# Kernel tuning notes

Measured on AMD Instinct MI355X. Metric: run time of the kernel, lower is better.

## Reference

```python
import jax, jax.numpy as jnp
import numpy as np

N, K, B, D, T = 30000, 32, 8, 256, 10
NC = T + 1            # int_small_classes
LB_COL, UB_COL = 21, 22
INF = 1e18


def _ln(x, g, b, eps=1e-5):
    m = jnp.mean(x, axis=-1, keepdims=True)
    v = jnp.mean((x - m) ** 2, axis=-1, keepdims=True)
    return (x - m) * jax.lax.rsqrt(v + eps) * g + b


def _head(x, ng, nb, W1, b1, W2, b2, Wh, bh):
    # LayerNorm -> Linear -> GELU -> Linear -> GELU -> residual -> head (dropout off: eval)
    h = _ln(x, ng, nb)
    h = jax.nn.gelu(h @ W1.T + b1, approximate=False)
    h = jax.nn.gelu(h @ W2.T + b2, approximate=False)
    return (x + h) @ Wh.T + bh


def setup_inputs():
    key = jax.random.key(0)
    ks = jax.random.split(key, 32)
    s = 0.05
    inp = {}
    inp['evolved_tokens'] = jax.random.normal(ks[0], (B * K, D), jnp.float32)
    inp['var_batch'] = jnp.sort(jax.random.randint(ks[1], (N,), 0, B))
    aw = jax.random.uniform(ks[2], (N, K), jnp.float32)
    inp['attn_weights'] = aw / aw.sum(-1, keepdims=True)
    inp['var_types'] = jax.random.randint(ks[3], (N,), 0, 3)
    inp['z_var_0'] = jax.random.normal(ks[4], (N, D), jnp.float32)
    vf = 0.1 * jax.random.normal(ks[5], (N, 23), jnp.float32)
    lb = jnp.floor(jax.random.uniform(ks[6], (N,), minval=-5.0, maxval=0.0))
    ub = lb + jnp.floor(jax.random.uniform(ks[7], (N,), minval=0.0, maxval=30.0))
    ub = jnp.where(jax.random.uniform(ks[8], (N,)) < 0.1, 1e19, ub)
    inp['variable_features'] = vf.at[:, LB_COL].set(lb).at[:, UB_COL].set(ub)
    # deslice proj + fusion norm
    inp['Wp'] = s * jax.random.normal(ks[9], (D, D), jnp.float32)
    inp['bp'] = jnp.zeros((D,), jnp.float32)
    inp['fn_g'] = jnp.ones((D,), jnp.float32)
    inp['fn_b'] = jnp.zeros((D,), jnp.float32)
    # three decoder heads
    i = 10
    for name, out in (('bin', 1), ('ints', NC), ('intl', 1)):
        inp[name + '_ng'] = jnp.ones((D,), jnp.float32)
        inp[name + '_nb'] = jnp.zeros((D,), jnp.float32)
        inp[name + '_W1'] = s * jax.random.normal(ks[i], (D, D), jnp.float32)
        inp[name + '_b1'] = jnp.zeros((D,), jnp.float32)
        inp[name + '_W2'] = s * jax.random.normal(ks[i + 1], (D, D), jnp.float32)
        inp[name + '_b2'] = jnp.zeros((D,), jnp.float32)
        inp[name + '_Wh'] = s * jax.random.normal(ks[i + 2], (out, D), jnp.float32)
        inp[name + '_bh'] = (jnp.full((out,), -0.5, jnp.float32) if name == 'bin'
                             else jnp.zeros((out,), jnp.float32))
        i += 3
    return inp


def reference(evolved_tokens, var_batch, attn_weights, var_types, z_var_0,
              variable_features, Wp, bp, fn_g, fn_b,
              bin_ng, bin_nb, bin_W1, bin_b1, bin_W2, bin_b2, bin_Wh, bin_bh,
              ints_ng, ints_nb, ints_W1, ints_b1, ints_W2, ints_b2, ints_Wh, ints_bh,
              intl_ng, intl_nb, intl_W1, intl_b1, intl_W2, intl_b2, intl_Wh, intl_bh):
    # 1. deslice: attn_weights @ projected evolved tokens of the variable's graph
    proj = evolved_tokens @ Wp.T + bp          # [B*K, D]
    tok3 = proj.reshape(B, K, D)
    z_des = jnp.einsum('nk,nkd->nd', attn_weights, tok3[var_batch])  # [N, D]
    # 2. residual fusion + LayerNorm
    z_out = _ln(z_des + z_var_0, fn_g, fn_b)
    # 3. routing (extract_int_routing)
    lb = variable_features[:, LB_COL]
    ub = variable_features[:, UB_COL]
    is_int = var_types == 2
    finite = (jnp.abs(lb) < INF) & (jnp.abs(ub) < INF)
    mask_int_small = is_int & finite & ((ub - lb) <= T)
    mask_int_large = is_int & ~mask_int_small
    mask_bin = var_types == 1
    offsets = jnp.floor(lb)                                   # [N]
    ranges = jnp.clip(jnp.ceil(ub) - offsets + 1.0, 1.0, NC).astype(jnp.int32)  # [N]
    # 4. decode. Heads are evaluated densely on all N rows; the original's
    #    gather->MLP->scatter equals row-selection of these dense outputs.
    prob_bin = jax.nn.sigmoid(_head(z_out, bin_ng, bin_nb, bin_W1, bin_b1,
                                    bin_W2, bin_b2, bin_Wh, bin_bh))   # [N, 1]
    logits = _head(z_out, ints_ng, ints_nb, ints_W1, ints_b1,
                   ints_W2, ints_b2, ints_Wh, ints_bh)                 # [N, NC]
    valid = jnp.arange(NC)[None, :] < ranges[:, None]
    logits = jnp.where(valid, logits, -1e9)  # dynamic logit masking of invalid classes
    pred_large = _head(z_out, intl_ng, intl_nb, intl_W1, intl_b1,
                       intl_W2, intl_b2, intl_Wh, intl_bh)             # [N, 1]
    return (z_out, prob_bin, logits, pred_large,
            mask_bin, mask_int_small, mask_int_large, offsets, ranges)
```

## Files before the change

kernel.cpp:

```cpp
#include <hip/hip_runtime.h>
#include <math.h>

#define NV   30000
#define DD   256
#define KK   32
#define NCLS 11
#define NT   469
#define NTZ  938

#define OZ  0
#define OPB 7680000
#define OLG 7710000
#define OPL 8040000
#define OMB 8070000
#define OMS 8100000
#define OML 8130000
#define OOF 8160000
#define ORG 8190000

typedef __bf16 bf16x8 __attribute__((ext_vector_type(8)));
typedef float  f32x4  __attribute__((ext_vector_type(4)));

__device__ __forceinline__ unsigned short f2b(float f) {
    unsigned u = __float_as_uint(f);
    u += 0x7fffu + ((u >> 16) & 1u);
    return (unsigned short)(u >> 16);
}

__device__ __forceinline__ float gelu_f(float x) {
    float x2 = x * x;
    float m = x * __builtin_fmaf(-0.0713548163f, x2, -1.5957691216f);
    float e = __expf(m);
    return x * __builtin_amdgcn_rcpf(1.0f + e);
}

__device__ __forceinline__ int swz(int row) { return (row + (row >> 3)) & 7; }
__device__ __forceinline__ int lidx(int row, int col) {
    return row * 256 + ((((col) >> 3) ^ swz(row)) << 3) + (col & 7);
}
__device__ __forceinline__ int physchunk(int ck, int row) {
    return (ck & ~7) | ((ck & 7) ^ swz(row));
}
__device__ __forceinline__ int pswz(int o, int n) { return n ^ (((o >> 2) & 3) << 4); }

struct WP {
    const float *W1, *ng, *nb, *b1, *W2, *Wh;
    unsigned short *W1e, *W2b, *Whb;
    float *b1e, *swh;
    int nc;
};

__global__ void k_prep(const float* __restrict__ et, const float* __restrict__ Wp,
                       const float* __restrict__ bp, unsigned short* __restrict__ projT,
                       const float* __restrict__ vf, const int* __restrict__ vt,
                       float* __restrict__ out,
                       WP wa, WP wb, WP wc) {
    __shared__ float es[DD];
    __shared__ float red[4], red2[4];
    if (blockIdx.y == 0) {
        int r = blockIdx.x, c = threadIdx.x;
        es[c] = et[r * DD + c];
        __syncthreads();
        const float4* w4 = (const float4*)(Wp + c * DD);
        float a0 = 0.f, a1 = 0.f, a2 = 0.f, a3 = 0.f;
#pragma unroll 16
        for (int d = 0; d < DD / 4; ++d) {
            float4 w = w4[d];
            a0 += es[4 * d] * w.x;
            a1 += es[4 * d + 1] * w.y;
            a2 += es[4 * d + 2] * w.z;
            a3 += es[4 * d + 3] * w.w;
        }
        float acc = bp[c] + ((a0 + a1) + (a2 + a3));
        projT[c * DD + r] = f2b(acc);
        return;
    }
    if (blockIdx.y == 4) {
        int n = blockIdx.x * 256 + threadIdx.x;
        if (n < NV) {
            float lb = vf[n * 23 + 21], ub = vf[n * 23 + 22];
            int t = vt[n];
            bool is_int = (t == 2);
            bool finite = (fabsf(lb) < 1e18f) && (fabsf(ub) < 1e18f);
            bool small_ = is_int && finite && (ub - lb <= 10.0f);
            float off = floorf(lb);
            float rngf = ceilf(ub) - off + 1.0f;
            rngf = fminf(fmaxf(rngf, 1.0f), (float)NCLS);
            out[OMB + n] = (t == 1) ? 1.0f : 0.0f;
            out[OMS + n] = small_ ? 1.0f : 0.0f;
            out[OML + n] = (is_int && !small_) ? 1.0f : 0.0f;
            out[OOF + n] = off;
            out[ORG + n] = (float)((int)rngf);
        }
        return;
    }
    WP wp = (blockIdx.y == 1) ? wa : ((blockIdx.y == 2) ? wb : wc);
    int j = blockIdx.x, d = threadIdx.x;
    float v1 = wp.W1[j * DD + d];
    wp.W1e[j * DD + d] = f2b(v1 * wp.ng[d]);
    wp.W2b[j * DD + d] = f2b(wp.W2[j * DD + d]);
    float p2 = 0.f;
    if (j < 16) {
        p2 = (j < wp.nc) ? wp.Wh[j * DD + d] : 0.f;
        wp.Whb[j * DD + d] = f2b(p2);
    }
    float p = v1 * wp.nb[d];
#pragma unroll
    for (int m = 1; m < 64; m <<= 1) { p += __shfl_xor(p, m); p2 += __shfl_xor(p2, m); }
    if ((d & 63) == 0) { red[d >> 6] = p; red2[d >> 6] = p2; }
    __syncthreads();
    if (d == 0) {
        wp.b1e[j] = wp.b1[j] + red[0] + red[1] + red[2] + red[3];
        if (j < 16) wp.swh[j] = red2[0] + red2[1] + red2[2] + red2[3];
    }
}

__global__ __launch_bounds__(512)
void k_zout(const unsigned short* __restrict__ projT, const int* __restrict__ vb,
            const float* __restrict__ aw, const float* __restrict__ z0,
            const float* __restrict__ g, const float* __restrict__ b,
            const unsigned short* __restrict__ Whb, const float* __restrict__ swh,
            float* __restrict__ out, unsigned short* __restrict__ zhat,
            float* __restrict__ zwhT) {
    __shared__ unsigned short Al[32 * 256];
    __shared__ float sqs[32 * 8], sqq[32 * 8];
    __shared__ float mvm[32], mvr[32], sig[32];
    __shared__ float gs[DD], bs[DD];
    __shared__ float swhs[48];
    int tid = threadIdx.x;
    int lane = tid & 63, wv = tid >> 6;
    int l15 = lane & 15, lq = lane >> 4;
    int n0 = blockIdx.x * 32;
    int sadd = (blockIdx.x & 1) << 2;

    int bmin = vb[n0];
    int bmax = vb[(n0 + 31 < NV) ? (n0 + 31) : (NV - 1)];

    if (tid < 256) gs[tid] = g[tid];
    else           bs[tid - 256] = b[tid - 256];
    if (tid < 48) swhs[tid] = swh[tid];
    {
        uint4 z4 = make_uint4(0, 0, 0, 0);
        uint4* dst = (uint4*)Al;
        dst[tid] = z4;
        dst[tid + 512] = z4;
    }
    __syncthreads();
    if (tid < 256) {
        int r = tid >> 3, sub = tid & 7;
        int n = n0 + r;
        if (n < NV) {
            int bb = vb[n];
            float4 a4 = *(const float4*)(aw + (size_t)n * KK + sub * 4);
            int j0 = bb * 32 + sub * 4;
            int ck = j0 >> 3;
            int chunk = (ck & ~7) | ((ck & 7) ^ ((swz(r) + sadd) & 7));
            int phys = r * 256 + (chunk << 3) + (j0 & 7);
            ushort4 u;
            u.x = f2b(a4.x); u.y = f2b(a4.y); u.z = f2b(a4.z); u.w = f2b(a4.w);
            *(ushort4*)(Al + phys) = u;
        }
    }
    __syncthreads();

    int nb0 = wv * 32;
    f32x4 acc[2][2];
#pragma unroll
    for (int mt = 0; mt < 2; ++mt)
#pragma unroll
        for (int nt = 0; nt < 2; ++nt) acc[mt][nt] = f32x4{0.f, 0.f, 0.f, 0.f};

    {
        const unsigned short* Bb = projT + (size_t)(nb0 + l15) * DD + lq * 8;
        for (int ks = bmin; ks <= bmax; ++ks) {
            bf16x8 bfr[2];
#pragma unroll
            for (int nt = 0; nt < 2; ++nt)
                bfr[nt] = *(const bf16x8*)(Bb + nt * 16 * DD + ks * 32);
            int ck = ks * 4 + lq;
#pragma unroll
            for (int mt = 0; mt < 2; ++mt) {
                int row = mt * 16 + l15;
                int chunk = (ck & ~7) | ((ck & 7) ^ ((swz(row) + sadd) & 7));
                bf16x8 afr = *(const bf16x8*)(Al + row * 256 + (chunk << 3));
#pragma unroll
                for (int nt = 0; nt < 2; ++nt)
                    acc[mt][nt] = __builtin_amdgcn_mfma_f32_16x16x32_bf16(afr, bfr[nt], acc[mt][nt], 0, 0, 0);
            }
        }
    }
#pragma unroll
    for (int mt = 0; mt < 2; ++mt)
#pragma unroll
        for (int nt = 0; nt < 2; ++nt) {
            int col = nb0 + nt * 16 + l15;
#pragma unroll
            for (int r = 0; r < 4; ++r) {
                int n = n0 + mt * 16 + lq * 4 + r;
                float zv = (n < NV) ? z0[(size_t)n * DD + col] : 0.f;
                acc[mt][nt][r] += zv;
            }
        }
#pragma unroll
    for (int mt = 0; mt < 2; ++mt)
#pragma unroll
        for (int r = 0; r < 4; ++r) {
            float s = acc[mt][0][r] + acc[mt][1][r];
            float q = acc[mt][0][r] * acc[mt][0][r] + acc[mt][1][r] * acc[mt][1][r];
#pragma unroll
            for (int m = 1; m < 16; m <<= 1) { s += __shfl_xor(s, m); q += __shfl_xor(q, m); }
            if (l15 == 0) { int row = mt * 16 + lq * 4 + r; sqs[row * 8 + wv] = s; sqq[row * 8 + wv] = q; }
        }
    __syncthreads();
    if (tid < 32) {
        float s = 0.f, q = 0.f;
#pragma unroll
        for (int w = 0; w < 8; ++w) { s += sqs[tid * 8 + w]; q += sqq[tid * 8 + w]; }
        float mean = s * (1.f / DD);
        float var  = q * (1.f / DD) - mean * mean;
        mvm[tid] = mean; mvr[tid] = rsqrtf(var + 1e-5f);
    }
    __syncthreads();
#pragma unroll
    for (int mt = 0; mt < 2; ++mt)
#pragma unroll
        for (int nt = 0; nt < 2; ++nt) {
            int col = nb0 + nt * 16 + l15;
#pragma unroll
            for (int r = 0; r < 4; ++r) {
                int row = mt * 16 + lq * 4 + r;
                float z = (acc[mt][nt][r] - mvm[row]) * mvr[row] * gs[col] + bs[col];
                acc[mt][nt][r] = z;
                int n = n0 + row;
                if (n < NV) out[OZ + (size_t)n * DD + col] = z;
            }
        }
#pragma unroll
    for (int mt = 0; mt < 2; ++mt)
#pragma unroll
        for (int r = 0; r < 4; ++r) {
            float s = acc[mt][0][r] + acc[mt][1][r];
            float q = acc[mt][0][r] * acc[mt][0][r] + acc[mt][1][r] * acc[mt][1][r];
#pragma unroll
            for (int m = 1; m < 16; m <<= 1) { s += __shfl_xor(s, m); q += __shfl_xor(q, m); }
            if (l15 == 0) { int row = mt * 16 + lq * 4 + r; sqs[row * 8 + wv] = s; sqq[row * 8 + wv] = q; }
        }
    __syncthreads();
    if (tid < 32) {
        float s = 0.f, q = 0.f;
#pragma unroll
        for (int w = 0; w < 8; ++w) { s += sqs[tid * 8 + w]; q += sqq[tid * 8 + w]; }
        float m2 = s * (1.f / DD);
        float v2 = q * (1.f / DD) - m2 * m2;
        float r2 = rsqrtf(v2 + 1e-5f);
        mvm[tid] = m2; mvr[tid] = r2; sig[tid] = (v2 + 1e-5f) * r2;
    }
    __syncthreads();
#pragma unroll
    for (int mt = 0; mt < 2; ++mt)
#pragma unroll
        for (int nt = 0; nt < 2; ++nt) {
            int col = nb0 + nt * 16 + l15;
#pragma unroll
            for (int r = 0; r < 4; ++r) {
                int row = mt * 16 + lq * 4 + r;
                int idx = row * 256 + ((((col) >> 3) ^ ((swz(row) + sadd) & 7)) << 3) + (col & 7);
                Al[idx] = f2b((acc[mt][nt][r] - mvm[row]) * mvr[row]);
            }
        }
    __syncthreads();
    if (wv < 2) {
        f32x4 ac2[3];
#pragma unroll
        for (int mf = 0; mf < 3; ++mf) ac2[mf] = f32x4{0.f, 0.f, 0.f, 0.f};
        const unsigned short* Ab = Whb + (size_t)l15 * DD + lq * 8;
        int rowb = wv * 16 + l15;
        int sw = (swz(rowb) + sadd) & 7;
#pragma unroll
        for (int ks = 0; ks < 8; ++ks) {
            int ck = ks * 4 + lq;
            int chunk = (ck & ~7) | ((ck & 7) ^ sw);
            bf16x8 bb2 = *(const bf16x8*)(Al + rowb * 256 + (chunk << 3));
#pragma unroll
            for (int mf = 0; mf < 3; ++mf) {
                bf16x8 aa2 = *(const bf16x8*)(Ab + (size_t)mf * 16 * DD + ks * 32);
                ac2[mf] = __builtin_amdgcn_mfma_f32_16x16x32_bf16(aa2, bb2, ac2[mf], 0, 0, 0);
            }
        }
        int nl = wv * 16 + l15;
        float sg = sig[nl], mu = mvm[nl];
        int t64 = blockIdx.x >> 1, half = blockIdx.x & 1;
#pragma unroll
        for (int mf = 0; mf < 3; ++mf)
#pragma unroll
            for (int r = 0; r < 4; ++r) {
                int o = mf * 16 + lq * 4 + r;
                zwhT[(size_t)t64 * 3072 + o * 64 + half * 32 + nl] = sg * ac2[mf][r] + mu * swhs[o];
            }
    }
    {
        uint4* dstg = (uint4*)(zhat + (size_t)n0 * 256);
        const uint4* srcl = (const uint4*)Al;
        dstg[tid] = srcl[tid];
        dstg[tid + 512] = srcl[tid + 512];
    }
}

struct HeadP {
    const unsigned short *W1e, *W2b, *Whb;
    const float *b1e, *b2, *bh;
    int nc;
};

__global__ __launch_bounds__(512, 4)
void k_heads(const unsigned short* __restrict__ zhat, const float* __restrict__ zwhT,
             const float* __restrict__ ranges,
             HeadP h0, HeadP h1p, HeadP h2p,
             float* __restrict__ opb, float* __restrict__ olg, float* __restrict__ opl) {
    __shared__ unsigned short hl1[64 * 256];
    __shared__ unsigned short hl2[64 * 256];
    __shared__ float b1s[DD], b2s[DD];
    __shared__ float zws[16 * 64];
    __shared__ float rgs[64];
    __shared__ float bhs[16];

    int head = blockIdx.x / NT;
    int tile = blockIdx.x % NT;
    HeadP hp = (head == 0) ? h0 : ((head == 1) ? h1p : h2p);
    int nc = hp.nc;
    int n0 = tile * 64;
    int tid = threadIdx.x, lane = tid & 63, wv = tid >> 6;
    int l15 = lane & 15, lq = lane >> 4;
    int M0 = wv * 32;

    {
        const uint4* src = (const uint4*)(zhat + (size_t)n0 * 256);
        uint4* dst = (uint4*)hl1;
#pragma unroll
        for (int j = 0; j < 4; ++j) dst[tid + j * 512] = src[tid + j * 512];
    }
    if (tid < 256) b1s[tid] = hp.b1e[tid];
    else           b2s[tid - 256] = hp.b2[tid - 256];
    ((float2*)zws)[tid] = ((const float2*)(zwhT + (size_t)(tile * 3 + head) * 1024))[tid];
    if (tid < 64) { int n = n0 + tid; rgs[tid] = (n < NV) ? ranges[n] : 0.f; }
    else if (tid < 80) { int o = tid - 64; bhs[o] = (o < nc) ? hp.bh[o] : 0.f; }
    __syncthreads();

    const unsigned short* Ab1 = hp.W1e + (size_t)(M0 + l15) * DD + lq * 8;
    const unsigned short* Ab2 = hp.W2b + (size_t)(M0 + l15) * DD + lq * 8;

    f32x4 acc[2][4];
#pragma unroll
    for (int mt = 0; mt < 2; ++mt)
#pragma unroll
        for (int nt = 0; nt < 4; ++nt) acc[mt][nt] = f32x4{0.f, 0.f, 0.f, 0.f};

    bf16x8 afr[3][2];
#pragma unroll
    for (int mt = 0; mt < 2; ++mt) {
        afr[0][mt] = *(const bf16x8*)(Ab1 + mt * 16 * DD);
        afr[1][mt] = *(const bf16x8*)(Ab1 + mt * 16 * DD + 32);
    }

#pragma unroll
    for (int ks = 0; ks < 8; ++ks) {
        int cur = ks % 3;
        if (ks < 6) {
#pragma unroll
            for (int mt = 0; mt < 2; ++mt)
                afr[(ks + 2) % 3][mt] = *(const bf16x8*)(Ab1 + mt * 16 * DD + (ks + 2) * 32);
        }
        int ck = ks * 4 + lq;
        bf16x8 bfr[4];
#pragma unroll
        for (int nt = 0; nt < 4; ++nt) {
            int row = nt * 16 + l15;
            bfr[nt] = *(const bf16x8*)(hl1 + row * 256 + (physchunk(ck, row) << 3));
        }
#pragma unroll
        for (int nt = 0; nt < 4; ++nt)
#pragma unroll
            for (int mt = 0; mt < 2; ++mt)
                acc[mt][nt] = __builtin_amdgcn_mfma_f32_16x16x32_bf16(afr[cur][mt], bfr[nt], acc[mt][nt], 0, 0, 0);
    }

#pragma unroll
    for (int mt = 0; mt < 2; ++mt) {
        afr[0][mt] = *(const bf16x8*)(Ab2 + mt * 16 * DD);
        afr[1][mt] = *(const bf16x8*)(Ab2 + mt * 16 * DD + 32);
    }

#pragma unroll
    for (int mt = 0; mt < 2; ++mt) {
        int jb = M0 + mt * 16 + lq * 4;
        float4 bias = *(const float4*)(b1s + jb);
        int chunk = jb >> 3;
#pragma unroll
        for (int nt = 0; nt < 4; ++nt) {
            int n = nt * 16 + l15;
            ushort4 u;
            u.x = f2b(gelu_f(acc[mt][nt][0] + bias.x));
            u.y = f2b(gelu_f(acc[mt][nt][1] + bias.y));
            u.z = f2b(gelu_f(acc[mt][nt][2] + bias.z));
            u.w = f2b(gelu_f(acc[mt][nt][3] + bias.w));
            *(ushort4*)(hl2 + n * 256 + (physchunk(chunk, n) << 3) + (jb & 7)) = u;
        }
    }
    __syncthreads();

#pragma unroll
    for (int mt = 0; mt < 2; ++mt)
#pragma unroll
        for (int nt = 0; nt < 4; ++nt) acc[mt][nt] = f32x4{0.f, 0.f, 0.f, 0.f};
#pragma unroll
    for (int ks = 0; ks < 8; ++ks) {
        int cur = ks % 3;
        if (ks < 6) {
#pragma unroll
            for (int mt = 0; mt < 2; ++mt)
                afr[(ks + 2) % 3][mt] = *(const bf16x8*)(Ab2 + mt * 16 * DD + (ks + 2) * 32);
        }
        int ck = ks * 4 + lq;
        bf16x8 bfr[4];
#pragma unroll
        for (int nt = 0; nt < 4; ++nt) {
            int row = nt * 16 + l15;
            bfr[nt] = *(const bf16x8*)(hl2 + row * 256 + (physchunk(ck, row) << 3));
        }
#pragma unroll
        for (int nt = 0; nt < 4; ++nt)
#pragma unroll
            for (int mt = 0; mt < 2; ++mt)
                acc[mt][nt] = __builtin_amdgcn_mfma_f32_16x16x32_bf16(afr[cur][mt], bfr[nt], acc[mt][nt], 0, 0, 0);
    }

    bf16x8 apr = *(const bf16x8*)(hp.Whb + (size_t)l15 * DD + wv * 32 + lq * 8);

#pragma unroll
    for (int mt = 0; mt < 2; ++mt) {
        int jb = M0 + mt * 16 + lq * 4;
        float4 bias = *(const float4*)(b2s + jb);
        int chunk = jb >> 3;
#pragma unroll
        for (int nt = 0; nt < 4; ++nt) {
            int n = nt * 16 + l15;
            ushort4 u;
            u.x = f2b(gelu_f(acc[mt][nt][0] + bias.x));
            u.y = f2b(gelu_f(acc[mt][nt][1] + bias.y));
            u.z = f2b(gelu_f(acc[mt][nt][2] + bias.z));
            u.w = f2b(gelu_f(acc[mt][nt][3] + bias.w));
            *(ushort4*)(hl1 + n * 256 + (physchunk(chunk, n) << 3) + (jb & 7)) = u;
        }
    }
    __syncthreads();

    f32x4 ap[4];
#pragma unroll
    for (int nt = 0; nt < 4; ++nt) ap[nt] = f32x4{0.f, 0.f, 0.f, 0.f};
    {
        int ck = wv * 4 + lq;
#pragma unroll
        for (int nt = 0; nt < 4; ++nt) {
            int row = nt * 16 + l15;
            bf16x8 bfr = *(const bf16x8*)(hl1 + row * 256 + (physchunk(ck, row) << 3));
            ap[nt] = __builtin_amdgcn_mfma_f32_16x16x32_bf16(apr, bfr, ap[nt], 0, 0, 0);
        }
    }
    {
        float* pb = (float*)hl2;
#pragma unroll
        for (int nt = 0; nt < 4; ++nt)
#pragma unroll
            for (int r = 0; r < 4; ++r) {
                int o = lq * 4 + r;
                int n = nt * 16 + l15;
                pb[wv * 1024 + o * 64 + pswz(o, n)] = ap[nt][r];
            }
    }
    __syncthreads();

    const float* pb = (const float*)hl2;
    for (int idx = tid; idx < 64 * nc; idx += 512) {
        int o = idx >> 6, n = idx & 63;
        float val = bhs[o] + zws[o * 64 + n];
        int nsw = pswz(o, n);
#pragma unroll
        for (int w = 0; w < 8; ++w) val += pb[w * 1024 + o * 64 + nsw];
        int ng = n0 + n;
        if (ng < NV) {
            if (head == 0)      opb[ng] = __builtin_amdgcn_rcpf(1.f + __expf(-val));
            else if (head == 2) opl[ng] = val;
            else {
                int rng = (int)rgs[n];
                olg[(size_t)ng * NCLS + o] = (o < rng) ? val : -1e9f;
            }
        }
    }
}

extern "C" void kernel_launch(void* const* d_in, const int* in_sizes, int n_in,
                              void* d_out, int out_size, void* d_ws, size_t ws_size,
                              hipStream_t stream) {
    const float* et = (const float*)d_in[0];
    const int*   vb = (const int*)d_in[1];
    const float* aw = (const float*)d_in[2];
    const int*   vt = (const int*)d_in[3];
    const float* z0 = (const float*)d_in[4];
    const float* vf = (const float*)d_in[5];
    const float* Wp = (const float*)d_in[6];
    const float* bp = (const float*)d_in[7];
    const float* fg = (const float*)d_in[8];
    const float* fb = (const float*)d_in[9];
    float* out = (float*)d_out;

    char* ws = (char*)d_ws;
    unsigned short* projT = (unsigned short*)ws;
    float* b1e           = (float*)(ws + 131072);
    unsigned short* W1e  = (unsigned short*)(ws + 134144);
    unsigned short* W2b  = (unsigned short*)(ws + 527360);
    unsigned short* Whb  = (unsigned short*)(ws + 920576);
    float* swh           = (float*)(ws + 945152);
    float* zwhT          = (float*)(ws + 945408);
    unsigned short* zhat = (unsigned short*)(ws + 6708480);

    WP wps[3];
    for (int h = 0; h < 3; ++h) {
        wps[h].W1 = (const float*)d_in[12 + 8 * h];
        wps[h].ng = (const float*)d_in[10 + 8 * h];
        wps[h].nb = (const float*)d_in[11 + 8 * h];
        wps[h].b1 = (const float*)d_in[13 + 8 * h];
        wps[h].W2 = (const float*)d_in[14 + 8 * h];
        wps[h].Wh = (const float*)d_in[16 + 8 * h];
        wps[h].W1e = W1e + h * 65536;
        wps[h].W2b = W2b + h * 65536;
        wps[h].Whb = Whb + h * 4096;
        wps[h].b1e = b1e + h * 256;
        wps[h].swh = swh + h * 16;
        wps[h].nc  = (h == 1) ? NCLS : 1;
    }
    k_prep<<<dim3(256, 5), 256, 0, stream>>>(et, Wp, bp, projT, vf, vt, out,
                                             wps[0], wps[1], wps[2]);

    k_zout<<<NTZ, 512, 0, stream>>>(projT, vb, aw, z0, fg, fb, Whb, swh,
                                    out, zhat, zwhT);

    HeadP hps[3];
    for (int h = 0; h < 3; ++h) {
        hps[h].W1e = W1e + h * 65536;
        hps[h].W2b = W2b + h * 65536;
        hps[h].Whb = Whb + h * 4096;
        hps[h].b1e = b1e + h * 256;
        hps[h].b2  = (const float*)d_in[15 + 8 * h];
        hps[h].bh  = (const float*)d_in[17 + 8 * h];
        hps[h].nc  = (h == 1) ? NCLS : 1;
    }
    k_heads<<<3 * NT, 512, 0, stream>>>(zhat, zwhT, out + ORG,
                                        hps[0], hps[1], hps[2],
                                        out + OPB, out + OLG, out + OPL);
}
```

Measured before the change: 236.0 us.

## Stage MFMA output in LDS and run LayerNorm epilogue row-wise with float4 accesses

New measurement: 232.5 us. Within noise of the previous version (-1.5%).

```diff
diff --git a/kernel.cpp b/kernel.cpp
--- a/kernel.cpp
+++ b/kernel.cpp
@@ -7,6 +7,7 @@
 #define NCLS 11
 #define NT   469
 #define NTZ  938
+#define ZFS  260
 
 #define OZ  0
 #define OPB 7680000
@@ -35,9 +36,6 @@
 }
 
 __device__ __forceinline__ int swz(int row) { return (row + (row >> 3)) & 7; }
-__device__ __forceinline__ int lidx(int row, int col) {
-    return row * 256 + ((((col) >> 3) ^ swz(row)) << 3) + (col & 7);
-}
 __device__ __forceinline__ int physchunk(int ck, int row) {
     return (ck & ~7) | ((ck & 7) ^ swz(row));
 }
@@ -123,7 +121,8 @@
             float* __restrict__ out, unsigned short* __restrict__ zhat,
             float* __restrict__ zwhT) {
     __shared__ unsigned short Al[32 * 256];
-    __shared__ float sqs[32 * 8], sqq[32 * 8];
+    __shared__ float Zf[32 * ZFS];
+    __shared__ float sA[32], qA[32];
     __shared__ float mvm[32], mvr[32], sig[32];
     __shared__ float gs[DD], bs[DD];
     __shared__ float swhs[48];
@@ -196,79 +195,87 @@
             int col = nb0 + nt * 16 + l15;
 #pragma unroll
             for (int r = 0; r < 4; ++r) {
-                int n = n0 + mt * 16 + lq * 4 + r;
-                float zv = (n < NV) ? z0[(size_t)n * DD + col] : 0.f;
-                acc[mt][nt][r] += zv;
+                int row = mt * 16 + lq * 4 + r;
+                Zf[row * ZFS + col] = acc[mt][nt][r];
             }
         }
-#pragma unroll
-    for (int mt = 0; mt < 2; ++mt)
-#pragma unroll
-        for (int r = 0; r < 4; ++r) {
-            float s = acc[mt][0][r] + acc[mt][1][r];
-            float q = acc[mt][0][r] * acc[mt][0][r] + acc[mt][1][r] * acc[mt][1][r];
-#pragma unroll
-            for (int m = 1; m < 16; m <<= 1) { s += __shfl_xor(s, m); q += __shfl_xor(q, m); }
-            if (l15 == 0) { int row = mt * 16 + lq * 4 + r; sqs[row * 8 + wv] = s; sqq[row * 8 + wv] = q; }
-        }
+    __syncthreads();
+
+#pragma unroll
+    for (int i = 0; i < 4; ++i) {
+        int token = wv + i * 8;
+        int n = n0 + token;
+        float4 zv = make_float4(0.f, 0.f, 0.f, 0.f);
+        if (n < NV) zv = *(const float4*)(z0 + (size_t)n * DD + lane * 4);
+        float* zr = Zf + token * ZFS + lane * 4;
+        float4 v = *(float4*)zr;
+        v.x += zv.x; v.y += zv.y; v.z += zv.z; v.w += zv.w;
+        *(float4*)zr = v;
+        float s = (v.x + v.y) + (v.z + v.w);
+        float q = v.x * v.x + v.y * v.y + v.z * v.z + v.w * v.w;
+#pragma unroll
+        for (int m = 1; m < 64; m <<= 1) { s += __shfl_xor(s, m); q += __shfl_xor(q, m); }
+        if (lane == 0) { sA[token] = s; qA[token] = q; }
+    }
     __syncthreads();
     if (tid < 32) {
-        float s = 0.f, q = 0.f;
-#pragma unroll
-        for (int w = 0; w < 8; ++w) { s += sqs[tid * 8 + w]; q += sqq[tid * 8 + w]; }
-        float mean = s * (1.f / DD);
-        float var  = q * (1.f / DD) - mean * mean;
+        float mean = sA[tid] * (1.f / DD);
+        float var  = qA[tid] * (1.f / DD) - mean * mean;
         mvm[tid] = mean; mvr[tid] = rsqrtf(var + 1e-5f);
     }
     __syncthreads();
-#pragma unroll
-    for (int mt = 0; mt < 2; ++mt)
-#pragma unroll
-        for (int nt = 0; nt < 2; ++nt) {
-            int col = nb0 + nt * 16 + l15;
-#pragma unroll
-            for (int r = 0; r < 4; ++r) {
-                int row = mt * 16 + lq * 4 + r;
-                float z = (acc[mt][nt][r] - mvm[row]) * mvr[row] * gs[col] + bs[col];
-                acc[mt][nt][r] = z;
-                int n = n0 + row;
-                if (n < NV) out[OZ + (size_t)n * DD + col] = z;
-            }
-        }
-#pragma unroll
-    for (int mt = 0; mt < 2; ++mt)
-#pragma unroll
-        for (int r = 0; r < 4; ++r) {
-            float s = acc[mt][0][r] + acc[mt][1][r];
-            float q = acc[mt][0][r] * acc[mt][0][r] + acc[mt][1][r] * acc[mt][1][r];
-#pragma unroll
-            for (int m = 1; m < 16; m <<= 1) { s += __shfl_xor(s, m); q += __shfl_xor(q, m); }
-            if (l15 == 0) { int row = mt * 16 + lq * 4 + r; sqs[row * 8 + wv] = s; sqq[row * 8 + wv] = q; }
-        }
+
+#pragma unroll
+    for (int i = 0; i < 4; ++i) {
+        int token = wv + i * 8;
+        int n = n0 + token;
+        float* zr = Zf + token * ZFS + lane * 4;
+        float4 v = *(float4*)zr;
+        float m = mvm[token], rr = mvr[token];
+        const float4 g4 = *(const float4*)(gs + lane * 4);
+        const float4 b4 = *(const float4*)(bs + lane * 4);
+        float4 z;
+        z.x = (v.x - m) * rr * g4.x + b4.x;
+        z.y = (v.y - m) * rr * g4.y + b4.y;
+        z.z = (v.z - m) * rr * g4.z + b4.z;
+        z.w = (v.w - m) * rr * g4.w + b4.w;
+        if (n < NV) *(float4*)(out + OZ + (size_t)n * DD + lane * 4) = z;
+        *(float4*)zr = z;
+        float s = (z.x + z.y) + (z.z + z.w);
+        float q = z.x * z.x + z.y * z.y + z.z * z.z + z.w * z.w;
+#pragma unroll
+        for (int m2_ = 1; m2_ < 64; m2_ <<= 1) { s += __shfl_xor(s, m2_); q += __shfl_xor(q, m2_); }
+        if (lane == 0) { sA[token] = s; qA[token] = q; }
+    }
     __syncthreads();
     if (tid < 32) {
-        float s = 0.f, q = 0.f;
-#pragma unroll
-        for (int w = 0; w < 8; ++w) { s += sqs[tid * 8 + w]; q += sqq[tid * 8 + w]; }
-        float m2 = s * (1.f / DD);
-        float v2 = q * (1.f / DD) - m2 * m2;
+        float m2 = sA[tid] * (1.f / DD);
+        float v2 = qA[tid] * (1.f / DD) - m2 * m2;
         float r2 = rsqrtf(v2 + 1e-5f);
         mvm[tid] = m2; mvr[tid] = r2; sig[tid] = (v2 + 1e-5f) * r2;
     }
     __syncthreads();
-#pragma unroll
-    for (int mt = 0; mt < 2; ++mt)
-#pragma unroll
-        for (int nt = 0; nt < 2; ++nt) {
-            int col = nb0 + nt * 16 + l15;
-#pragma unroll
-            for (int r = 0; r < 4; ++r) {
-                int row = mt * 16 + lq * 4 + r;
-                int idx = row * 256 + ((((col) >> 3) ^ ((swz(row) + sadd) & 7)) << 3) + (col & 7);
-                Al[idx] = f2b((acc[mt][nt][r] - mvm[row]) * mvr[row]);
-            }
-        }
-    __syncthreads();
+
+#pragma unroll
+    for (int i = 0; i < 4; ++i) {
+        int token = wv + i * 8;
+        int c4 = lane * 4;
+        const float* zr = Zf + token * ZFS + c4;
+        float4 z = *(const float4*)zr;
+        float m = mvm[token], rr = mvr[token];
+        ushort4 u;
+        u.x = f2b((z.x - m) * rr);
+        u.y = f2b((z.y - m) * rr);
+        u.z = f2b((z.z - m) * rr);
+        u.w = f2b((z.w - m) * rr);
+        int ck = c4 >> 3;
+        int chunk = (ck & ~7) | ((ck & 7) ^ ((swz(token) + sadd) & 7));
+        int off = (chunk << 3) + (c4 & 7);
+        *(ushort4*)(Al + token * 256 + off) = u;
+        *(ushort4*)(zhat + (size_t)(n0 + token) * 256 + off) = u;
+    }
+    __syncthreads();
+
     if (wv < 2) {
         f32x4 ac2[3];
 #pragma unroll
@@ -297,12 +304,6 @@
                 int o = mf * 16 + lq * 4 + r;
                 zwhT[(size_t)t64 * 3072 + o * 64 + half * 32 + nl] = sg * ac2[mf][r] + mu * swhs[o];
             }
-    }
-    {
-        uint4* dstg = (uint4*)(zhat + (size_t)n0 * 256);
-        const uint4* srcl = (const uint4*)Al;
-        dstg[tid] = srcl[tid];
-        dstg[tid + 512] = srcl[tid + 512];
     }
 }
 
```
